# Kernel optimization log

Hardware: AMD Instinct MI355X
Metric: run time of the kernel (lower is better)

## Reference

```python
import jax, jax.numpy as jnp
import numpy as np

N = 23
B = 16384
T = 12


def setup_inputs() -> dict:
    key = jax.random.key(0)
    k1, k2, k3 = jax.random.split(key, 3)
    flow_x = jax.random.normal(k1, (B, N, N, T), dtype=jnp.float32)
    adj = jax.random.randint(k2, (N, N), 0, 2).astype(jnp.int32)
    W = jax.random.uniform(k3, (N, N, N), dtype=jnp.float32)
    return {"flow_x": flow_x, "adj": adj, "W": W}


def reference(flow_x, adj, W):
    # data = flow_x[:, :, :, -1]  -> (B, N, N), last time step
    data = flow_x[..., -1]
    # force self-loops: adj[i][i] = 1
    adj = adj.at[jnp.diag_indices(N)].set(1)
    # shift each row of W so its minimum is >= 0 (only if min < 0)
    mn = jnp.min(W, axis=-1, keepdims=True)          # (N, N, 1)
    mn = jnp.minimum(mn, 0.0)                         # where(min>0, 0, min)
    attention = W - mn                                # (N, N, N)
    # zero out attention[:, i, j] wherever adj[i, j] == 0 (mask over dims 1,2)
    mask = (adj != 0).astype(attention.dtype)         # (N, N)
    attention = attention * mask[None, :, :]
    # row-normalize over last dim
    attention = attention / jnp.sum(attention, axis=-1, keepdims=True)
    # original: x[b, i, :] = attention[i] @ data[b, :, i]
    # x[b, i, k] = sum_m attention[i, k, m] * data[b, m, i]
    x = jnp.einsum('ikm,bmi->bik', attention, data)   # (B, N, N)
    return x[..., None]                               # (B, N, N, 1)
```

## Files before the change

kernel.cpp:

```cpp
#include <hip/hip_runtime.h>

#define N 23
#define NN 529
#define TT 12
#define BPB 8
#define THREADS 256
#define DATA_LD 24
#define DATA_BSTRIDE (N * DATA_LD)
#define STG ((BPB * NN + THREADS - 1) / THREADS)

typedef float f4 __attribute__((ext_vector_type(4)));

__device__ __forceinline__ void compute_arow(int r, const int* __restrict__ adj,
                                             const float* __restrict__ W, float* a) {
    int i = r / N;
    int k = r - i * N;
    const float* wrow = W + r * N;
    float mn = 0.f;
#pragma unroll
    for (int m = 0; m < N; ++m) { a[m] = wrow[m]; mn = fminf(mn, a[m]); }
    float s = 0.f;
#pragma unroll
    for (int m = 0; m < N; ++m) {
        int msk = (m == k) ? 1 : adj[k * N + m];
        float x = (msk != 0) ? (a[m] - mn) : 0.f;
        a[m] = x;
        s += x;
    }
    float inv = 1.f / s;
#pragma unroll
    for (int m = 0; m < N; ++m) a[m] *= inv;
}

__device__ __forceinline__ void emit_row(int r, const float* a, const float* data,
                                         float* __restrict__ out, int bbase) {
    int i = r / N;
    const float* drow0 = data + i * DATA_LD;
#pragma unroll
    for (int bl = 0; bl < BPB; ++bl) {
        const f4* d = (const f4*)(drow0 + bl * DATA_BSTRIDE);
        f4 d0 = d[0], d1 = d[1], d2 = d[2], d3 = d[3], d4 = d[4], d5 = d[5];
        float acc = a[0] * d0.x;
        acc = fmaf(a[1],  d0.y, acc);
        acc = fmaf(a[2],  d0.z, acc);
        acc = fmaf(a[3],  d0.w, acc);
        acc = fmaf(a[4],  d1.x, acc);
        acc = fmaf(a[5],  d1.y, acc);
        acc = fmaf(a[6],  d1.z, acc);
        acc = fmaf(a[7],  d1.w, acc);
        acc = fmaf(a[8],  d2.x, acc);
        acc = fmaf(a[9],  d2.y, acc);
        acc = fmaf(a[10], d2.z, acc);
        acc = fmaf(a[11], d2.w, acc);
        acc = fmaf(a[12], d3.x, acc);
        acc = fmaf(a[13], d3.y, acc);
        acc = fmaf(a[14], d3.z, acc);
        acc = fmaf(a[15], d3.w, acc);
        acc = fmaf(a[16], d4.x, acc);
        acc = fmaf(a[17], d4.y, acc);
        acc = fmaf(a[18], d4.z, acc);
        acc = fmaf(a[19], d4.w, acc);
        acc = fmaf(a[20], d5.x, acc);
        acc = fmaf(a[21], d5.y, acc);
        acc = fmaf(a[22], d5.z, acc);
        __builtin_nontemporal_store(acc, out + (size_t)(bbase + bl) * NN + r);
    }
}

__global__ __launch_bounds__(THREADS) void fused_gat(const float* __restrict__ flow,
                                                     const int* __restrict__ adj,
                                                     const float* __restrict__ W,
                                                     float* __restrict__ out) {
    __shared__ float data[BPB * DATA_BSTRIDE];
    const int tid = threadIdx.x;
    const int bbase = (gridDim.x - 1 - blockIdx.x) * BPB;

    float sv[STG];
    int laddr[STG];
#pragma unroll
    for (int it = 0; it < STG; ++it) {
        int idx = tid + it * THREADS;
        bool ok = (idx < BPB * NN);
        int idc = ok ? idx : 0;
        int bl = idc / NN;
        int r = idc - bl * NN;
        int m = r / N;
        int i = r - m * N;
        const f4* src = (const f4*)(flow + (size_t)(bbase + bl) * (NN * TT))
                        + (m * (N * TT / 4) + i * 3 + 2);
        f4 v = __builtin_nontemporal_load(src);
        sv[it] = v.w;
        laddr[it] = ok ? (bl * DATA_BSTRIDE + i * DATA_LD + m) : -1;
    }

    float a0[N];
    compute_arow(tid, adj, W, a0);

#pragma unroll
    for (int it = 0; it < STG; ++it)
        if (laddr[it] >= 0) data[laddr[it]] = sv[it];
    __syncthreads();

    emit_row(tid, a0, data, out, bbase);

    {
        float a1[N];
        compute_arow(tid + THREADS, adj, W, a1);
        emit_row(tid + THREADS, a1, data, out, bbase);
    }
    if (tid < NN - 2 * THREADS) {
        float a2[N];
        compute_arow(tid + 2 * THREADS, adj, W, a2);
        emit_row(tid + 2 * THREADS, a2, data, out, bbase);
    }
}

extern "C" void kernel_launch(void* const* d_in, const int* in_sizes, int n_in,
                              void* d_out, int out_size, void* d_ws, size_t ws_size,
                              hipStream_t stream) {
    const float* flow = (const float*)d_in[0];
    const int* adj = (const int*)d_in[1];
    const float* W = (const float*)d_in[2];
    float* out = (float*)d_out;

    const int B = in_sizes[0] / (NN * TT);

    fused_gat<<<B / BPB, THREADS, 0, stream>>>(flow, adj, W, out);
}
```

Before: 543.5 us.

## Stage last-timestep data into LDS via global_load_lds direct DMA

Result: slower. 570.3 us (+4.9%).

```diff
diff --git a/kernel.cpp b/kernel.cpp
--- a/kernel.cpp
+++ b/kernel.cpp
@@ -1,4 +1,5 @@
 #include <hip/hip_runtime.h>
+#include <stdint.h>
 
 #define N 23
 #define NN 529
@@ -7,13 +8,15 @@
 #define THREADS 256
 #define DATA_LD 24
 #define DATA_BSTRIDE (N * DATA_LD)
-#define STG ((BPB * NN + THREADS - 1) / THREADS)
+#define SLOTS (BPB * DATA_BSTRIDE)
+#define DMA_ITERS ((SLOTS + THREADS - 1) / THREADS)
 
-typedef float f4 __attribute__((ext_vector_type(4)));
+#define AS1 __attribute__((address_space(1)))
+#define AS3 __attribute__((address_space(3)))
 
 __device__ __forceinline__ void compute_arow(int r, const int* __restrict__ adj,
                                              const float* __restrict__ W, float* a) {
-    int i = r / N;
+    int i = (unsigned)r / N;
     int k = r - i * N;
     const float* wrow = W + r * N;
     float mn = 0.f;
@@ -34,71 +37,46 @@
 
 __device__ __forceinline__ void emit_row(int r, const float* a, const float* data,
                                          float* __restrict__ out, int bbase) {
-    int i = r / N;
-    const float* drow0 = data + i * DATA_LD;
+    const int i = (unsigned)r / N;
 #pragma unroll
     for (int bl = 0; bl < BPB; ++bl) {
-        const f4* d = (const f4*)(drow0 + bl * DATA_BSTRIDE);
-        f4 d0 = d[0], d1 = d[1], d2 = d[2], d3 = d[3], d4 = d[4], d5 = d[5];
-        float acc = a[0] * d0.x;
-        acc = fmaf(a[1],  d0.y, acc);
-        acc = fmaf(a[2],  d0.z, acc);
-        acc = fmaf(a[3],  d0.w, acc);
-        acc = fmaf(a[4],  d1.x, acc);
-        acc = fmaf(a[5],  d1.y, acc);
-        acc = fmaf(a[6],  d1.z, acc);
-        acc = fmaf(a[7],  d1.w, acc);
-        acc = fmaf(a[8],  d2.x, acc);
-        acc = fmaf(a[9],  d2.y, acc);
-        acc = fmaf(a[10], d2.z, acc);
-        acc = fmaf(a[11], d2.w, acc);
-        acc = fmaf(a[12], d3.x, acc);
-        acc = fmaf(a[13], d3.y, acc);
-        acc = fmaf(a[14], d3.z, acc);
-        acc = fmaf(a[15], d3.w, acc);
-        acc = fmaf(a[16], d4.x, acc);
-        acc = fmaf(a[17], d4.y, acc);
-        acc = fmaf(a[18], d4.z, acc);
-        acc = fmaf(a[19], d4.w, acc);
-        acc = fmaf(a[20], d5.x, acc);
-        acc = fmaf(a[21], d5.y, acc);
-        acc = fmaf(a[22], d5.z, acc);
+        const float* d = data + bl * DATA_BSTRIDE + i;
+        float acc = a[0] * d[0];
+#pragma unroll
+        for (int m = 1; m < N; ++m) acc = fmaf(a[m], d[m * DATA_LD], acc);
         __builtin_nontemporal_store(acc, out + (size_t)(bbase + bl) * NN + r);
     }
 }
 
-__global__ __launch_bounds__(THREADS) void fused_gat(const float* __restrict__ flow,
-                                                     const int* __restrict__ adj,
-                                                     const float* __restrict__ W,
-                                                     float* __restrict__ out) {
-    __shared__ float data[BPB * DATA_BSTRIDE];
+__global__ __launch_bounds__(THREADS, 8) void fused_gat(const float* __restrict__ flow,
+                                                        const int* __restrict__ adj,
+                                                        const float* __restrict__ W,
+                                                        float* __restrict__ out) {
+    __shared__ float data[SLOTS];
     const int tid = threadIdx.x;
     const int bbase = (gridDim.x - 1 - blockIdx.x) * BPB;
 
-    float sv[STG];
-    int laddr[STG];
 #pragma unroll
-    for (int it = 0; it < STG; ++it) {
-        int idx = tid + it * THREADS;
-        bool ok = (idx < BPB * NN);
-        int idc = ok ? idx : 0;
-        int bl = idc / NN;
-        int r = idc - bl * NN;
-        int m = r / N;
-        int i = r - m * N;
-        const f4* src = (const f4*)(flow + (size_t)(bbase + bl) * (NN * TT))
-                        + (m * (N * TT / 4) + i * 3 + 2);
-        f4 v = __builtin_nontemporal_load(src);
-        sv[it] = v.w;
-        laddr[it] = ok ? (bl * DATA_BSTRIDE + i * DATA_LD + m) : -1;
+    for (int it = 0; it < DMA_ITERS; ++it) {
+        const unsigned s = (unsigned)tid + it * THREADS;
+        const unsigned wbase = s & ~63u;
+        if (wbase + 64 <= SLOTS) {
+            const unsigned bl = s / DATA_BSTRIDE;
+            const unsigned rr = s - bl * DATA_BSTRIDE;
+            const unsigned m  = rr / DATA_LD;
+            const unsigned i4 = rr - m * DATA_LD;
+            const float* src = (i4 < N)
+                ? flow + ((size_t)(bbase + bl) * (NN * TT) + m * (N * TT) + i4 * TT + (TT - 1))
+                : flow;
+            __builtin_amdgcn_global_load_lds((const AS1 unsigned int*)src,
+                                             (AS3 unsigned int*)(data + wbase),
+                                             4, 0, 0);
+        }
     }
 
     float a0[N];
     compute_arow(tid, adj, W, a0);
 
-#pragma unroll
-    for (int it = 0; it < STG; ++it)
-        if (laddr[it] >= 0) data[laddr[it]] = sv[it];
     __syncthreads();
 
     emit_row(tid, a0, data, out, bbase);
```
